# Kernel tuning notes

Hardware: AMD Instinct MI355X
Metric: run time of the kernel (lower is better)

Reference implementation:

```python
import jax, jax.numpy as jnp
import numpy as np

HEADS = 12
D_MODEL = 768
D_K = D_MODEL // HEADS


def setup_inputs() -> dict:
    key = jax.random.key(0)
    ks = jax.random.split(key, 11)
    B, S, D = 2, 2048, D_MODEL
    s = 1.0 / np.sqrt(D)
    return {
        "query": jax.random.normal(ks[0], (B, S, D), jnp.float32),
        "key": jax.random.normal(ks[1], (B, S, D), jnp.float32),
        "value": jax.random.normal(ks[2], (B, S, D), jnp.float32),
        "Wq": jax.random.normal(ks[3], (D, D), jnp.float32) * s,
        "bq": jnp.zeros((D,), jnp.float32),
        "Wk": jax.random.normal(ks[4], (D, D), jnp.float32) * s,
        "bk": jnp.zeros((D,), jnp.float32),
        "Wv": jax.random.normal(ks[5], (D, D), jnp.float32) * s,
        "bv": jnp.zeros((D,), jnp.float32),
        "Wo": jax.random.normal(ks[6], (D, D), jnp.float32) * s,
        "bo": jnp.zeros((D,), jnp.float32),
    }


def reference(query, key, value, Wq, bq, Wk, bk, Wv, bv, Wo, bo):
    B, S, D = query.shape
    # linear projections (weights stored as [in, out])
    q = query @ Wq + bq
    k = key @ Wk + bk
    v = value @ Wv + bv
    # [B, H, S, d_k]
    q = q.reshape(B, S, HEADS, D_K).transpose(0, 2, 1, 3)
    k = k.reshape(B, S, HEADS, D_K).transpose(0, 2, 1, 3)
    v = v.reshape(B, S, HEADS, D_K).transpose(0, 2, 1, 3)
    # scores: note module scales by sqrt(d_k) (key.size(-1)), not self.scaled
    scores = jnp.einsum("bhqd,bhkd->bhqk", q, k) / jnp.sqrt(jnp.asarray(D_K, q.dtype))
    weights = jax.nn.softmax(scores, axis=-1)
    context = jnp.einsum("bhqk,bhkd->bhqd", weights, v)
    context = context.transpose(0, 2, 1, 3).reshape(B, S, D)
    return context @ Wo + bo
```

## Files before the change

kernel.cpp:

```cpp
#include <hip/hip_runtime.h>
#include <hip/hip_bf16.h>
#include <math.h>

#define D_MODEL 768
#define HEADS 12
#define DK 64
#define SEQ 2048
#define BATCH 2
#define MTOT (BATCH * SEQ)
#define QSCALE 0.18033688011112042f

using short8 = __attribute__((ext_vector_type(8))) short;
using us4    = __attribute__((ext_vector_type(4))) unsigned short;
using f32x4  = __attribute__((ext_vector_type(4))) float;
using f32x16 = __attribute__((ext_vector_type(16))) float;

static __device__ __forceinline__ unsigned f2bf2(float x, float y) {
    __hip_bfloat162 t = __float22bfloat162_rn(float2{x, y});
    return *reinterpret_cast<unsigned*>(&t);
}
static __device__ __forceinline__ unsigned short f2bf1(float x) {
    __hip_bfloat16 t = __float2bfloat16(x);
    return *reinterpret_cast<unsigned short*>(&t);
}
static __device__ __forceinline__ float bf2f(unsigned short u) {
    unsigned v = (unsigned)u << 16;
    return __uint_as_float(v);
}
static __device__ __forceinline__ short8 cvt8(float4 a, float4 b) {
    union { unsigned u[4]; short8 s; } r;
    r.u[0] = f2bf2(a.x, a.y);
    r.u[1] = f2bf2(a.z, a.w);
    r.u[2] = f2bf2(b.x, b.y);
    r.u[3] = f2bf2(b.z, b.w);
    return r.s;
}
static __device__ __forceinline__ float fast_exp2(float x) {
#if __has_builtin(__builtin_amdgcn_exp2f)
    return __builtin_amdgcn_exp2f(x);
#else
    return __expf(x * 0.6931471805599453f);
#endif
}
static __device__ __forceinline__ unsigned pk2(float lo, float hi) {
    unsigned d;
    asm("v_cvt_pk_bf16_f32 %0, %1, %2" : "=v"(d) : "v"(lo), "v"(hi));
    return d;
}

static __device__ __forceinline__ void gload_lds16(const void* g, void* l) {
    __builtin_amdgcn_global_load_lds(
        (const __attribute__((address_space(1))) void*)g,
        (__attribute__((address_space(3))) void*)l, 16, 0, 0);
}

static __device__ __forceinline__ void barrier_lgkm() {
    asm volatile("s_waitcnt lgkmcnt(0)" ::: "memory");
    __builtin_amdgcn_s_barrier();
    __builtin_amdgcn_sched_barrier(0);
}
static __device__ __forceinline__ void barrier_vm0() {
    asm volatile("s_waitcnt vmcnt(0)" ::: "memory");
    __builtin_amdgcn_s_barrier();
    __builtin_amdgcn_sched_barrier(0);
}

__global__ __launch_bounds__(256) void cvt_wt_k(
    const float* __restrict__ Wq, const float* __restrict__ Wk,
    const float* __restrict__ Wv, const float* __restrict__ Wo,
    unsigned short* __restrict__ Wqt, unsigned short* __restrict__ Wkt,
    unsigned short* __restrict__ Wvt, unsigned short* __restrict__ Wot)
{
    const int z = blockIdx.z;
    const float* W = z == 0 ? Wq : z == 1 ? Wk : z == 2 ? Wv : Wo;
    unsigned short* Wt = z == 0 ? Wqt : z == 1 ? Wkt : z == 2 ? Wvt : Wot;
    __shared__ float t[32][33];
    const int n0 = blockIdx.x * 32, k0 = blockIdx.y * 32;
    const int tx = threadIdx.x & 31;
    const int ty0 = (threadIdx.x >> 5) * 4;
    #pragma unroll
    for (int j = 0; j < 4; ++j)
        t[ty0 + j][tx] = W[(size_t)(k0 + ty0 + j) * D_MODEL + n0 + tx];
    __syncthreads();
    #pragma unroll
    for (int j = 0; j < 4; ++j)
        Wt[(size_t)(n0 + ty0 + j) * D_MODEL + k0 + tx] = f2bf1(t[tx][ty0 + j]);
}

__global__ __launch_bounds__(512) void gemm_qkv_k(
    const float* __restrict__ query, const float* __restrict__ key,
    const float* __restrict__ value,
    const unsigned short* __restrict__ Wqt, const unsigned short* __restrict__ Wkt,
    const unsigned short* __restrict__ Wvt,
    const float* __restrict__ bq, const float* __restrict__ bk,
    const float* __restrict__ bv,
    unsigned short* __restrict__ qb, unsigned short* __restrict__ kb,
    unsigned short* __restrict__ vb)
{
    __shared__ __align__(16) char gsm[65536];

    const int bid = blockIdx.x;
    const int xcd = bid & 7;
    const int idx = bid >> 3;
    const int z   = idx / 24;
    const int rr  = idx % 24;
    const int brow = (xcd * 4 + rr / 6) * 128;
    const int bcol = (rr % 6) * 128;

    const float* A           = z == 0 ? query : z == 1 ? key : value;
    const unsigned short* Wt = z == 0 ? Wqt : z == 1 ? Wkt : Wvt;
    const float* bias        = z == 0 ? bq  : z == 1 ? bk  : bv;
    unsigned short* C        = z == 0 ? qb  : z == 1 ? kb  : vb;
    const float scale        = z == 0 ? QSCALE : 1.0f;

    const int tid  = threadIdx.x;
    const int w    = tid >> 6;
    const int lane = tid & 63;
    const int g    = lane >> 4, c = lane & 15;
    const int wr   = w >> 2, wc = w & 3;

    f32x4 acc[4][2] = {};

    const int xc  = (c & 7) << 4;
    const int rb0 = c * 128 + ((g * 16) ^ xc);
    const int rb1 = c * 128 + ((64 + g * 16) ^ xc);

    int bsrow[2], bsoff[2], bsdst[2];
    #pragma unroll
    for (int r = 0; r < 2; ++r) {
        int phys = (w * 2 + r) * 1024 + lane * 16;
        int row  = phys >> 7;
        int slot = (phys >> 4) & 7;
        bsrow[r] = row;
        bsoff[r] = (slot ^ (row & 7)) * 8;
        bsdst[r] = (w * 2 + r) * 1024;
    }
    const int ar = tid >> 2;
    const int ac = (tid & 3) << 4;
    int awa[2];
    #pragma unroll
    for (int i = 0; i < 2; ++i)
        awa[i] = ar * 128 + (((ac << 1) + 16 * i) ^ ((ar & 7) << 4));
    const float* Ap32 = A + (size_t)(brow + ar) * D_MODEL + ac;

    float4 ra0, ra1, ra2, ra3;

    auto stageB = [&](int k0, int buf) {
        #pragma unroll
        for (int r = 0; r < 2; ++r)
            gload_lds16(Wt + (size_t)(bcol + bsrow[r]) * D_MODEL + k0 + bsoff[r],
                        gsm + 32768 + buf * 16384 + bsdst[r]);
    };
    auto loadA32 = [&](int k0) {
        ra0 = *(const float4*)(Ap32 + k0);
        ra1 = *(const float4*)(Ap32 + k0 + 4);
        ra2 = *(const float4*)(Ap32 + k0 + 8);
        ra3 = *(const float4*)(Ap32 + k0 + 12);
    };
    auto writeA32 = [&](int buf) {
        *(short8*)(gsm + buf * 16384 + awa[0]) = cvt8(ra0, ra1);
        *(short8*)(gsm + buf * 16384 + awa[1]) = cvt8(ra2, ra3);
    };

    stageB(0, 0);
    loadA32(0);
    writeA32(0);
    barrier_lgkm();

    for (int k0 = 0; k0 < D_MODEL; k0 += 128) {
        #pragma unroll
        for (int u = 0; u < 2; ++u) {
            const int kn = min(k0 + u * 64 + 64, D_MODEL - 64);
            stageB(kn, u ^ 1);
            loadA32(kn);
            __builtin_amdgcn_sched_barrier(0);

            __builtin_amdgcn_s_setprio(1);
            #pragma unroll
            for (int kstep = 0; kstep < 2; ++kstep) {
                const int rb = kstep ? rb1 : rb0;
                short8 af[4], bf[2];
                #pragma unroll
                for (int m = 0; m < 4; ++m)
                    af[m] = *(const short8*)(gsm + u * 16384 + wr * 8192 +
                                             m * 2048 + rb);
                #pragma unroll
                for (int n = 0; n < 2; ++n)
                    bf[n] = *(const short8*)(gsm + 32768 + u * 16384 +
                                             wc * 4096 + n * 2048 + rb);
                #pragma unroll
                for (int m = 0; m < 4; ++m)
                    #pragma unroll
                    for (int n = 0; n < 2; ++n)
                        acc[m][n] = __builtin_amdgcn_mfma_f32_16x16x32_bf16(
                                        af[m], bf[n], acc[m][n], 0, 0, 0);
            }
            __builtin_amdgcn_s_setprio(0);

            writeA32(u ^ 1);
            barrier_lgkm();
        }
    }

    #pragma unroll
    for (int m = 0; m < 4; ++m)
        #pragma unroll
        for (int n = 0; n < 2; ++n) {
            const int col = bcol + wc * 32 + n * 16 + c;
            const float bval = bias[col];
            #pragma unroll
            for (int j = 0; j < 4; ++j) {
                const int row = brow + wr * 64 + m * 16 + g * 4 + j;
                C[(size_t)row * D_MODEL + col] = f2bf1((acc[m][n][j] + bval) * scale);
            }
        }
}

__global__ __launch_bounds__(256) void gemm_o_k(
    const unsigned short* __restrict__ A, const unsigned short* __restrict__ Wt,
    const float* __restrict__ bias, float* __restrict__ C)
{
    __shared__ __align__(16) char gsm[32768];

    const int bid = blockIdx.x;
    const int xcd = bid & 7;
    const int idx = bid >> 3;
    const int brow = (xcd * 8 + idx / 12) * 64;
    const int bcol = (idx % 12) * 64;

    const int tid  = threadIdx.x;
    const int w    = tid >> 6;
    const int lane = tid & 63;
    const int g    = lane >> 4, c = lane & 15;
    const int wr   = w >> 1, wc = w & 1;

    f32x4 acc[2][2] = {{f32x4{0,0,0,0}, f32x4{0,0,0,0}},
                       {f32x4{0,0,0,0}, f32x4{0,0,0,0}}};

    const int xc  = (c & 7) << 4;
    const int rb0 = c * 128 + ((g * 16) ^ xc);
    const int rb1 = c * 128 + ((64 + g * 16) ^ xc);
    const int a0 = rb0 + wr * 4096, a1 = rb1 + wr * 4096;
    const int b0r = rb0 + 16384 + wc * 4096, b1r = rb1 + 16384 + wc * 4096;

    int bsrow[2], bsoff[2], bsdst[2];
    #pragma unroll
    for (int r = 0; r < 2; ++r) {
        int phys = (w + 4 * r) * 1024 + lane * 16;
        int row  = phys >> 7;
        int slot = (phys >> 4) & 7;
        bsrow[r] = row;
        bsoff[r] = (slot ^ (row & 7)) * 8;
        bsdst[r] = (w + 4 * r) * 1024;
    }

    auto stage = [&](int k0, int buf) {
        #pragma unroll
        for (int r = 0; r < 2; ++r) {
            gload_lds16(A  + (size_t)(brow + bsrow[r]) * D_MODEL + k0 + bsoff[r],
                        gsm + buf * 8192 + bsdst[r]);
            gload_lds16(Wt + (size_t)(bcol + bsrow[r]) * D_MODEL + k0 + bsoff[r],
                        gsm + 16384 + buf * 8192 + bsdst[r]);
        }
    };

    stage(0, 0);
    barrier_vm0();

    for (int k0 = 0; k0 < D_MODEL; k0 += 128) {
        #pragma unroll
        for (int u = 0; u < 2; ++u) {
            const int kn = min(k0 + u * 64 + 64, D_MODEL - 64);
            stage(kn, u ^ 1);
            __builtin_amdgcn_sched_barrier(0);

            #pragma unroll
            for (int kstep = 0; kstep < 2; ++kstep) {
                short8 af[2], bf[2];
                #pragma unroll
                for (int m = 0; m < 2; ++m)
                    af[m] = *(const short8*)(gsm + u * 8192 + m * 2048 +
                                             (kstep ? a1 : a0));
                #pragma unroll
                for (int n = 0; n < 2; ++n)
                    bf[n] = *(const short8*)(gsm + u * 8192 + n * 2048 +
                                             (kstep ? b1r : b0r));
                #pragma unroll
                for (int m = 0; m < 2; ++m)
                    #pragma unroll
                    for (int n = 0; n < 2; ++n)
                        acc[m][n] = __builtin_amdgcn_mfma_f32_16x16x32_bf16(
                                        af[m], bf[n], acc[m][n], 0, 0, 0);
            }
            barrier_vm0();
        }
    }

    #pragma unroll
    for (int m = 0; m < 2; ++m)
        #pragma unroll
        for (int n = 0; n < 2; ++n) {
            const int col = bcol + wc * 32 + n * 16 + c;
            const float bval = bias[col];
            #pragma unroll
            for (int j = 0; j < 4; ++j) {
                const int row = brow + wr * 32 + m * 16 + g * 4 + j;
                C[(size_t)row * D_MODEL + col] = acc[m][n][j] + bval;
            }
        }
}

__global__ __launch_bounds__(256) void attn_mfma_k(
    const unsigned short* __restrict__ q, const unsigned short* __restrict__ k,
    const unsigned short* __restrict__ v, unsigned short* __restrict__ opart,
    float* __restrict__ mpart, float* __restrict__ lpart)
{
    __shared__ __align__(16) char sm[32768];

    const int tid  = threadIdx.x;
    const int w    = tid >> 6;
    const int lane = tid & 63;
    const int c    = lane & 31;
    const int hi   = lane >> 5;

    const int bid  = blockIdx.x;
    const int swz  = (bid & 7) * 96 + (bid >> 3);
    const int qt   = swz & 15;
    const int rest = swz >> 4;
    const int half = rest & 1;
    const int hb   = rest >> 1;
    const int h    = hb % HEADS;
    const int b    = hb / HEADS;
    const int q0   = qt * 128;
    const int NT2  = 16;

    short8 qf[4];
    {
        const unsigned short* qp =
            q + (size_t)(b * SEQ + q0 + w * 32 + c) * D_MODEL + h * DK;
        #pragma unroll
        for (int t = 0; t < 4; ++t)
            qf[t] = *(const short8*)(qp + t * 16 + hi * 8);
    }

    float m_run = -INFINITY;
    f32x16 lacc = {};
    f32x16 o0 = {}, o1 = {};
    const short8 ONES = {0x3F80, 0x3F80, 0x3F80, 0x3F80,
                         0x3F80, 0x3F80, 0x3F80, 0x3F80};

    const int xc = (c & 7) << 4;
    int koff[4];
    #pragma unroll
    for (int t = 0; t < 4; ++t)
        koff[t] = ((32 * t + 16 * hi) ^ xc) + c * 128;

    int kdst[2];
    const unsigned short* kg[2];
    {
        const unsigned short* kbase =
            k + (size_t)(b * SEQ + half * (SEQ / 2)) * D_MODEL + h * DK;
        #pragma unroll
        for (int r = 0; r < 2; ++r) {
            int phys = (w + 4 * r) * 1024 + lane * 16;
            int row  = phys >> 7;
            int slot = (phys >> 4) & 7;
            kdst[r]  = (w + 4 * r) * 1024;
            kg[r]    = kbase + (size_t)row * D_MODEL + (slot ^ (row & 7)) * 8;
        }
    }
    const int cv = tid & 15, vd0 = (tid >> 4) << 2;
    const int vposP = 16 * (cv >> 3) + 8 * ((cv >> 2) & 1) + 2 * (cv & 3);
    int vwa[4];
    #pragma unroll
    for (int j = 0; j < 4; ++j) {
        const int row = vd0 + j;
        vwa[j] = 16384 + row * 128 + ((2 * vposP) ^ ((row & 7) << 4));
    }
    const unsigned short* vg =
        v + (size_t)(b * SEQ + half * (SEQ / 2) + cv) * D_MODEL + h * DK + vd0;
    const int TS = 64 * D_MODEL;

    us4 va, vb_, vc, vd;

    auto issue_k = [&](int buf) {
        gload_lds16(kg[0], sm + buf * 8192 + kdst[0]);
        gload_lds16(kg[1], sm + buf * 8192 + kdst[1]);
        kg[0] += TS; kg[1] += TS;
    };
    auto load_v = [&]() {
        va  = *(const us4*)(vg);
        vb_ = *(const us4*)(vg + 16 * D_MODEL);
        vc  = *(const us4*)(vg + 32 * D_MODEL);
        vd  = *(const us4*)(vg + 48 * D_MODEL);
        vg += TS;
    };
    auto write_v = [&](int buf) {
        #pragma unroll
        for (int j = 0; j < 4; ++j) {
            unsigned lo  = (unsigned)va[j]  | ((unsigned)vc[j] << 16);
            unsigned hi2 = (unsigned)vb_[j] | ((unsigned)vd[j] << 16);
            *(unsigned*)(sm + buf * 8192 + vwa[j])        = lo;
            *(unsigned*)(sm + buf * 8192 + (vwa[j] ^ 64)) = hi2;
        }
    };

    issue_k(0);
    __builtin_amdgcn_sched_barrier(0);
    load_v();
    write_v(0);
    barrier_lgkm();

    for (int kt2 = 0; kt2 < NT2; kt2 += 2) {
        #pragma unroll
        for (int u = 0; u < 2; ++u) {
            const int tile = kt2 + u;
            issue_k(u ^ 1);
            __builtin_amdgcn_sched_barrier(0);
            load_v();
            __builtin_amdgcn_sched_barrier(0);

            f32x16 s0 = {}, s1 = {};
            __builtin_amdgcn_s_setprio(1);
            #pragma unroll
            for (int t = 0; t < 4; ++t) {
                short8 kf0 = *(const short8*)(sm + u * 8192 + koff[t]);
                short8 kf1 = *(const short8*)(sm + u * 8192 + 4096 + koff[t]);
                s0 = __builtin_amdgcn_mfma_f32_32x32x16_bf16(kf0, qf[t], s0, 0, 0, 0);
                s1 = __builtin_amdgcn_mfma_f32_32x32x16_bf16(kf1, qf[t], s1, 0, 0, 0);
            }
            __builtin_amdgcn_s_setprio(0);

            float rmax = s0[0];
            #pragma unroll
            for (int r = 1; r < 16; ++r) rmax = fmaxf(rmax, s0[r]);
            #pragma unroll
            for (int r = 0; r < 16; ++r) rmax = fmaxf(rmax, s1[r]);
            rmax = fmaxf(rmax, __shfl_xor(rmax, 32));

            if (tile == 0) {
                m_run = rmax;
            } else if (__any(rmax > m_run + 11.0f)) {
                const float mnew = fmaxf(m_run, rmax);
                const float sc = fast_exp2(m_run - mnew);
                m_run = mnew;
                #pragma unroll
                for (int r = 0; r < 16; ++r) {
                    const float scr = __shfl(sc, (r & 3) + 8 * (r >> 2) + 4 * hi);
                    lacc[r] *= scr;
                    o0[r] *= scr;
                    o1[r] *= scr;
                }
            }

            #pragma unroll
            for (int r = 0; r < 16; ++r) {
                s0[r] = fast_exp2(s0[r] - m_run);
                s1[r] = fast_exp2(s1[r] - m_run);
            }

            __builtin_amdgcn_s_setprio(1);
            #pragma unroll
            for (int t = 0; t < 4; ++t) {
                union { unsigned u4[4]; short8 s8; } pf;
                #pragma unroll
                for (int j = 0; j < 4; ++j)
                    pf.u4[j] = pk2(s0[4 * t + j], s1[4 * t + j]);
                short8 vf0 = *(const short8*)(sm + 16384 + u * 8192 + koff[t]);
                short8 vf1 = *(const short8*)(sm + 16384 + u * 8192 + 4096 + koff[t]);
                lacc = __builtin_amdgcn_mfma_f32_32x32x16_bf16(pf.s8, ONES, lacc, 0, 0, 0);
                o0 = __builtin_amdgcn_mfma_f32_32x32x16_bf16(pf.s8, vf0, o0, 0, 0, 0);
                o1 = __builtin_amdgcn_mfma_f32_32x32x16_bf16(pf.s8, vf1, o1, 0, 0, 0);
            }
            __builtin_amdgcn_s_setprio(0);

            write_v(u ^ 1);
            barrier_lgkm();
        }
    }

    const size_t obase = (size_t)half * ((size_t)MTOT * D_MODEL) +
                         (size_t)(b * SEQ) * D_MODEL + h * DK;
    #pragma unroll
    for (int r = 0; r < 16; ++r) {
        const int qrow = q0 + w * 32 + (r & 3) + 8 * (r >> 2) + 4 * hi;
        unsigned short* ob = opart + obase + (size_t)qrow * D_MODEL;
        ob[c]      = f2bf1(o0[r]);
        ob[32 + c] = f2bf1(o1[r]);
    }
    const size_t mlbase = (size_t)half * MTOT * HEADS +
                          (size_t)(b * SEQ) * HEADS + h;
    if (hi == 0)
        mpart[mlbase + (size_t)(q0 + w * 32 + c) * HEADS] = m_run;
    if (c == 0) {
        #pragma unroll
        for (int r = 0; r < 16; ++r) {
            const int qrow = q0 + w * 32 + (r & 3) + 8 * (r >> 2) + 4 * hi;
            lpart[mlbase + (size_t)qrow * HEADS] = lacc[r];
        }
    }
}

__global__ __launch_bounds__(256) void combine_k(
    const unsigned short* __restrict__ op, const float* __restrict__ mp,
    const float* __restrict__ lp, unsigned short* __restrict__ cb)
{
    const int t   = blockIdx.x * 256 + threadIdx.x;
    const int row = t / 96;
    const int gi  = t - row * 96;
    const int col = gi << 3;
    const int h   = gi >> 3;

    const float m0 = mp[(size_t)row * HEADS + h];
    const float m1 = mp[(size_t)MTOT * HEADS + (size_t)row * HEADS + h];
    const float l0 = lp[(size_t)row * HEADS + h];
    const float l1 = lp[(size_t)MTOT * HEADS + (size_t)row * HEADS + h];
    const float m  = fmaxf(m0, m1);
    const float s0 = fast_exp2(m0 - m);
    const float s1 = fast_exp2(m1 - m);
    const float inv = 1.0f / (l0 * s0 + l1 * s1);
    const float a0 = s0 * inv, a1 = s1 * inv;

    const size_t off = (size_t)row * D_MODEL + col;
    us4 x0  = *(const us4*)(op + off);
    us4 x0b = *(const us4*)(op + off + 4);
    us4 x1  = *(const us4*)(op + (size_t)MTOT * D_MODEL + off);
    us4 x1b = *(const us4*)(op + (size_t)MTOT * D_MODEL + off + 4);

    union { unsigned short u[8]; short8 s; } r;
    #pragma unroll
    for (int j = 0; j < 4; ++j) {
        r.u[j]     = f2bf1(bf2f(x0[j])  * a0 + bf2f(x1[j])  * a1);
        r.u[4 + j] = f2bf1(bf2f(x0b[j]) * a0 + bf2f(x1b[j]) * a1);
    }
    *(short8*)(cb + off) = r.s;
}

extern "C" void kernel_launch(void* const* d_in, const int* in_sizes, int n_in,
                              void* d_out, int out_size, void* d_ws, size_t ws_size,
                              hipStream_t stream) {
    const float* query = (const float*)d_in[0];
    const float* key   = (const float*)d_in[1];
    const float* value = (const float*)d_in[2];
    const float* Wq = (const float*)d_in[3];
    const float* bq = (const float*)d_in[4];
    const float* Wk = (const float*)d_in[5];
    const float* bk = (const float*)d_in[6];
    const float* Wv = (const float*)d_in[7];
    const float* bv = (const float*)d_in[8];
    const float* Wo = (const float*)d_in[9];
    const float* bo = (const float*)d_in[10];
    float* out = (float*)d_out;

    const size_t mat = (size_t)MTOT * D_MODEL;
    unsigned short* qb  = (unsigned short*)d_ws;
    unsigned short* kb  = qb + mat;
    unsigned short* vb  = kb + mat;
    unsigned short* cb  = vb + mat;
    unsigned short* Wqt = cb + mat;
    unsigned short* Wkt = Wqt + (size_t)D_MODEL * D_MODEL;
    unsigned short* Wvt = Wkt + (size_t)D_MODEL * D_MODEL;
    unsigned short* Wot = Wvt + (size_t)D_MODEL * D_MODEL;
    unsigned short* op  = Wot + (size_t)D_MODEL * D_MODEL;
    float*          mp  = (float*)(op + 2 * mat);
    float*          lp  = mp + 2 * (size_t)MTOT * HEADS;

    cvt_wt_k<<<dim3(D_MODEL / 32, D_MODEL / 32, 4), 256, 0, stream>>>(
        Wq, Wk, Wv, Wo, Wqt, Wkt, Wvt, Wot);

    gemm_qkv_k<<<dim3(576), 512, 0, stream>>>(
        query, key, value, Wqt, Wkt, Wvt, bq, bk, bv, qb, kb, vb);

    attn_mfma_k<<<dim3(768), 256, 0, stream>>>(qb, kb, vb, op, mp, lp);

    combine_k<<<dim3(MTOT * D_MODEL / 8 / 256), 256, 0, stream>>>(op, mp, lp, cb);

    gemm_o_k<<<dim3(768), 256, 0, stream>>>(cb, Wot, bo, out);
}
```

Measured before the change: 104.8 us.

## Prefetch QKV projection tiles two stages ahead through registers instead of direct-to-LDS

```diff
diff --git a/kernel.cpp b/kernel.cpp
--- a/kernel.cpp
+++ b/kernel.cpp
@@ -12,6 +12,7 @@
 
 using short8 = __attribute__((ext_vector_type(8))) short;
 using us4    = __attribute__((ext_vector_type(4))) unsigned short;
+using us8    = __attribute__((ext_vector_type(8))) unsigned short;
 using f32x4  = __attribute__((ext_vector_type(4))) float;
 using f32x16 = __attribute__((ext_vector_type(16))) float;
 
@@ -125,16 +126,6 @@
     const int rb0 = c * 128 + ((g * 16) ^ xc);
     const int rb1 = c * 128 + ((64 + g * 16) ^ xc);
 
-    int bsrow[2], bsoff[2], bsdst[2];
-    #pragma unroll
-    for (int r = 0; r < 2; ++r) {
-        int phys = (w * 2 + r) * 1024 + lane * 16;
-        int row  = phys >> 7;
-        int slot = (phys >> 4) & 7;
-        bsrow[r] = row;
-        bsoff[r] = (slot ^ (row & 7)) * 8;
-        bsdst[r] = (w * 2 + r) * 1024;
-    }
     const int ar = tid >> 2;
     const int ac = (tid & 3) << 4;
     int awa[2];
@@ -143,36 +134,66 @@
         awa[i] = ar * 128 + (((ac << 1) + 16 * i) ^ ((ar & 7) << 4));
     const float* Ap32 = A + (size_t)(brow + ar) * D_MODEL + ac;
 
-    float4 ra0, ra1, ra2, ra3;
-
-    auto stageB = [&](int k0, int buf) {
-        #pragma unroll
-        for (int r = 0; r < 2; ++r)
-            gload_lds16(Wt + (size_t)(bcol + bsrow[r]) * D_MODEL + k0 + bsoff[r],
-                        gsm + 32768 + buf * 16384 + bsdst[r]);
-    };
-    auto loadA32 = [&](int k0) {
-        ra0 = *(const float4*)(Ap32 + k0);
-        ra1 = *(const float4*)(Ap32 + k0 + 4);
-        ra2 = *(const float4*)(Ap32 + k0 + 8);
-        ra3 = *(const float4*)(Ap32 + k0 + 12);
-    };
-    auto writeA32 = [&](int buf) {
-        *(short8*)(gsm + buf * 16384 + awa[0]) = cvt8(ra0, ra1);
-        *(short8*)(gsm + buf * 16384 + awa[1]) = cvt8(ra2, ra3);
-    };
-
-    stageB(0, 0);
-    loadA32(0);
-    writeA32(0);
+    const int br2 = tid >> 2;
+    const int bs2 = (tid & 3) << 1;
+    int bwa[2];
+    #pragma unroll
+    for (int i = 0; i < 2; ++i)
+        bwa[i] = 32768 + br2 * 128 + (((bs2 + i) ^ (br2 & 7)) << 4);
+    const unsigned short* WtB = Wt + (size_t)(bcol + br2) * D_MODEL + bs2 * 8;
+
+    float4 rA0[4], rA1[4];
+    us8    rB0[2], rB1[2];
+
+    auto loadA0 = [&](int k0) {
+        rA0[0] = *(const float4*)(Ap32 + k0);
+        rA0[1] = *(const float4*)(Ap32 + k0 + 4);
+        rA0[2] = *(const float4*)(Ap32 + k0 + 8);
+        rA0[3] = *(const float4*)(Ap32 + k0 + 12);
+    };
+    auto loadA1 = [&](int k0) {
+        rA1[0] = *(const float4*)(Ap32 + k0);
+        rA1[1] = *(const float4*)(Ap32 + k0 + 4);
+        rA1[2] = *(const float4*)(Ap32 + k0 + 8);
+        rA1[3] = *(const float4*)(Ap32 + k0 + 12);
+    };
+    auto loadB0 = [&](int k0) {
+        rB0[0] = *(const us8*)(WtB + k0);
+        rB0[1] = *(const us8*)(WtB + k0 + 8);
+    };
+    auto loadB1 = [&](int k0) {
+        rB1[0] = *(const us8*)(WtB + k0);
+        rB1[1] = *(const us8*)(WtB + k0 + 8);
+    };
+    auto writeA0 = [&](int buf) {
+        *(short8*)(gsm + buf * 16384 + awa[0]) = cvt8(rA0[0], rA0[1]);
+        *(short8*)(gsm + buf * 16384 + awa[1]) = cvt8(rA0[2], rA0[3]);
+    };
+    auto writeA1 = [&](int buf) {
+        *(short8*)(gsm + buf * 16384 + awa[0]) = cvt8(rA1[0], rA1[1]);
+        *(short8*)(gsm + buf * 16384 + awa[1]) = cvt8(rA1[2], rA1[3]);
+    };
+    auto writeB0 = [&](int buf) {
+        *(us8*)(gsm + buf * 16384 + bwa[0]) = rB0[0];
+        *(us8*)(gsm + buf * 16384 + bwa[1]) = rB0[1];
+    };
+    auto writeB1 = [&](int buf) {
+        *(us8*)(gsm + buf * 16384 + bwa[0]) = rB1[0];
+        *(us8*)(gsm + buf * 16384 + bwa[1]) = rB1[1];
+    };
+
+    loadA0(0);  loadB0(0);
+    loadA1(64); loadB1(64);
+    writeA0(0); writeB0(0);
     barrier_lgkm();
 
-    for (int k0 = 0; k0 < D_MODEL; k0 += 128) {
+    for (int iter = 0; iter < 6; ++iter) {
         #pragma unroll
         for (int u = 0; u < 2; ++u) {
-            const int kn = min(k0 + u * 64 + 64, D_MODEL - 64);
-            stageB(kn, u ^ 1);
-            loadA32(kn);
+            const int n   = 2 * iter + u;
+            const int kb2 = min(n + 2, 11) * 64;
+            if (u == 0) { loadA0(kb2); loadB0(kb2); }
+            else        { loadA1(kb2); loadB1(kb2); }
             __builtin_amdgcn_sched_barrier(0);
 
             __builtin_amdgcn_s_setprio(1);
@@ -185,19 +206,21 @@
                     af[m] = *(const short8*)(gsm + u * 16384 + wr * 8192 +
                                              m * 2048 + rb);
                 #pragma unroll
-                for (int n = 0; n < 2; ++n)
-                    bf[n] = *(const short8*)(gsm + 32768 + u * 16384 +
-                                             wc * 4096 + n * 2048 + rb);
+                for (int nn = 0; nn < 2; ++nn)
+                    bf[nn] = *(const short8*)(gsm + 32768 + u * 16384 +
+                                              wc * 4096 + nn * 2048 + rb);
                 #pragma unroll
                 for (int m = 0; m < 4; ++m)
                     #pragma unroll
-                    for (int n = 0; n < 2; ++n)
-                        acc[m][n] = __builtin_amdgcn_mfma_f32_16x16x32_bf16(
-                                        af[m], bf[n], acc[m][n], 0, 0, 0);
+                    for (int nn = 0; nn < 2; ++nn)
+                        acc[m][nn] = __builtin_amdgcn_mfma_f32_16x16x32_bf16(
+                                         af[m], bf[nn], acc[m][nn], 0, 0, 0);
             }
             __builtin_amdgcn_s_setprio(0);
-
-            writeA32(u ^ 1);
+            __builtin_amdgcn_sched_barrier(0);
+
+            if (u == 0) { writeA1(1); writeB1(1); }
+            else        { writeA0(0); writeB0(0); }
             barrier_lgkm();
         }
     }
```

Result: faster. 102.8 us (-2.0%).
